# Kernel tuning notes

Hardware: AMD Instinct MI355X
Metric: run time of the kernel (lower is better)

The kernel has to match this reference:

```python
import jax, jax.numpy as jnp
import numpy as np

M, N, DIM = 32, 32, 128
BATCH = 2048
NITER = 100
ALPHA = 0.3
SIGMA = max(M, N) / 2.0


def setup_inputs() -> dict:
    key = jax.random.key(0)
    k1, k2 = jax.random.split(key)
    x = jax.random.normal(k1, (BATCH, DIM), dtype=jnp.float32)
    weights = jax.random.normal(k2, (M * N, DIM), dtype=jnp.float32)
    # Grid locations exactly as in the torch module (meshgrid, ravel, transpose)
    xx, yy = np.meshgrid(np.linspace(0, M - 1, M), np.linspace(0, N - 1, N))
    locations = jnp.asarray(
        np.array((xx.ravel(), yy.ravel())).T.astype(np.int32)
    )  # [mn, 2]
    return {"x": x, "weights": weights, "locations": locations, "it": 5}


def reference(x, weights, locations, it):
    # --- BMU search: pairwise Euclidean distances weights [mn,d] vs x [b,d] ---
    # argmin over squared distances == argmin over cdist (sqrt is monotone)
    w2 = jnp.sum(weights * weights, axis=1)  # [mn]
    x2 = jnp.sum(x * x, axis=1)              # [b]
    d2 = w2[:, None] + x2[None, :] - 2.0 * (weights @ x.T)  # [mn, b]
    bmu_idx = jnp.argmin(d2, axis=0)         # [b]
    bmu_locs = locations[bmu_idx]            # [b, 2]

    # --- linearly decayed learning rate / neighbourhood width ---
    lr_decay = 1.0 - it / NITER
    alpha_op = ALPHA * lr_decay
    sigma_op = SIGMA * lr_decay

    # --- gaussian neighbourhood over grid distances: [mn, b] ---
    locf = locations.astype(jnp.float32)
    bmuf = bmu_locs.astype(jnp.float32)
    bmu_d2 = jnp.sum((locf[:, None, :] - bmuf[None, :, :]) ** 2, axis=2)  # [mn, b]
    lr_op = alpha_op * jnp.exp(-bmu_d2 / (sigma_op * sigma_op))           # [mn, b]

    # --- delta = sum_b lr_op[:, b] * (x[b] - w)  (algebraically reduced) ---
    # == lr_op @ x - rowsum(lr_op) * weights; avoids the [mn, b, d] intermediate
    delta = lr_op @ x - jnp.sum(lr_op, axis=1, keepdims=True) * weights  # [mn, d]
    return weights + delta
```

## Files before the change

kernel.cpp:

```cpp
#include <hip/hip_runtime.h>
#include <stdint.h>

#define DIM   128
#define MN    1024
#define BATCH 2048
#define ALPHA 0.3f
#define SIGMA 16.0f
#define LOG2E 1.44269504088896f

typedef _Float16 half8 __attribute__((ext_vector_type(8)));
typedef _Float16 half4 __attribute__((ext_vector_type(4)));
typedef float    floatx4 __attribute__((ext_vector_type(4)));


__global__ __launch_bounds__(256) void prep_kernel(
    const float* __restrict__ w, float* __restrict__ w2,
    _Float16* __restrict__ wh, _Float16* __restrict__ wl,
    float4* __restrict__ Sq)
{
  const int t = threadIdx.x;
  const int bid = blockIdx.x;
  if (bid < 8) {
    int idx = bid * 256 + t;
    int row = idx >> 1, half = idx & 1;
    int base = row * DIM + half * 64;
    float s = 0.f;
#pragma unroll
    for (int q = 0; q < 16; ++q) {
      float4 v = *reinterpret_cast<const float4*>(&w[base + q * 4]);
      s += v.x * v.x + v.y * v.y + v.z * v.z + v.w * v.w;
      half4 h, l;
      h[0] = (_Float16)v.x; l[0] = (_Float16)(v.x - (float)h[0]);
      h[1] = (_Float16)v.y; l[1] = (_Float16)(v.y - (float)h[1]);
      h[2] = (_Float16)v.z; l[2] = (_Float16)(v.z - (float)h[2]);
      h[3] = (_Float16)v.w; l[3] = (_Float16)(v.w - (float)h[3]);
      *reinterpret_cast<half4*>(&wh[base + q * 4]) = h;
      *reinterpret_cast<half4*>(&wl[base + q * 4]) = l;
    }
    s += __shfl_xor(s, 1);
    if (!half) w2[row] = s;
  } else {
    int i = (bid - 8) * 256 + t;
    Sq[i] = make_float4(0.f, 0.f, 0.f, 0.f);
  }
}

__global__ __launch_bounds__(512) void bmu_scatter_kernel(
    const float* __restrict__ x, const float* __restrict__ w2,
    const _Float16* __restrict__ wh, const _Float16* __restrict__ wl,
    float* __restrict__ S, float* __restrict__ cnt)
{
  __shared__ unsigned long long kb[8][16];
  __shared__ unsigned long long fkey[16];

  const int t    = threadIdx.x;
  const int lane = t & 63;
  const int wv   = t >> 6;
  const int b0   = blockIdx.x * 16;
  const int r    = lane & 15;
  const int q    = lane >> 4;

  half8 Bh[4], Bl[4];
  {
    const float* xr = x + (b0 + r) * DIM + q * 8;
#pragma unroll
    for (int c = 0; c < 4; ++c) {
      float4 v0 = *reinterpret_cast<const float4*>(xr + c * 32);
      float4 v1 = *reinterpret_cast<const float4*>(xr + c * 32 + 4);
      float xs[8] = {v0.x, v0.y, v0.z, v0.w, v1.x, v1.y, v1.z, v1.w};
#pragma unroll
      for (int j = 0; j < 8; ++j) {
        _Float16 h = (_Float16)xs[j];
        Bh[c][j] = h;
        Bl[c][j] = (_Float16)(xs[j] - (float)h);
      }
    }
  }

  unsigned long long kmin = ~0ull;
#pragma unroll 2
  for (int ut = 0; ut < 8; ++ut) {
    const int u0 = wv * 128 + ut * 16;
    const _Float16* wrh = wh + (u0 + r) * DIM + q * 8;
    const _Float16* wrl = wl + (u0 + r) * DIM + q * 8;
    half8 Ah[4], Al[4];
#pragma unroll
    for (int c = 0; c < 4; ++c) {
      Ah[c] = *reinterpret_cast<const half8*>(wrh + c * 32);
      Al[c] = *reinterpret_cast<const half8*>(wrl + c * 32);
    }
    floatx4 acc = {0.f, 0.f, 0.f, 0.f};
#pragma unroll
    for (int c = 0; c < 4; ++c) {
      acc = __builtin_amdgcn_mfma_f32_16x16x32_f16(Ah[c], Bh[c], acc, 0, 0, 0);
      acc = __builtin_amdgcn_mfma_f32_16x16x32_f16(Ah[c], Bl[c], acc, 0, 0, 0);
      acc = __builtin_amdgcn_mfma_f32_16x16x32_f16(Al[c], Bh[c], acc, 0, 0, 0);
    }
    float4 w2q = *reinterpret_cast<const float4*>(&w2[u0 + q * 4]);
    float w2a[4] = {w2q.x, w2q.y, w2q.z, w2q.w};
#pragma unroll
    for (int i = 0; i < 4; ++i) {
      float s = w2a[i] - 2.0f * acc[i];
      unsigned int sb = __float_as_uint(s);
      sb ^= (sb >> 31) ? 0xFFFFFFFFu : 0x80000000u;
      unsigned long long key =
          ((unsigned long long)sb << 32) | (unsigned int)(u0 + q * 4 + i);
      if (key < kmin) kmin = key;
    }
  }
  unsigned long long o;
  o = __shfl_xor(kmin, 16); if (o < kmin) kmin = o;
  o = __shfl_xor(kmin, 32); if (o < kmin) kmin = o;
  if (lane < 16) kb[wv][r] = kmin;
  __syncthreads();
  if (t < 16) {
    unsigned long long m = kb[0][t];
#pragma unroll
    for (int k = 1; k < 8; ++k)
      if (kb[k][t] < m) m = kb[k][t];
    fkey[t] = m;
  }
  __syncthreads();

  {
    int bl = t >> 5, cq = t & 31;
    unsigned int v = (unsigned int)fkey[bl];
    float4 xv = *reinterpret_cast<const float4*>(&x[(b0 + bl) * DIM + cq * 4]);
    float* Sv = S + v * DIM + cq * 4;
    unsafeAtomicAdd(&Sv[0], xv.x);
    unsafeAtomicAdd(&Sv[1], xv.y);
    unsafeAtomicAdd(&Sv[2], xv.z);
    unsafeAtomicAdd(&Sv[3], xv.w);
    if (cq == 0) unsafeAtomicAdd(&cnt[v], 1.0f);
  }
}

__global__ __launch_bounds__(512) void convfinal_kernel(
    const float* __restrict__ S, const float* __restrict__ cnt,
    const float* __restrict__ w, const int* __restrict__ itp,
    float* __restrict__ out)
{
  __shared__ float gxt[64], gyt[64];
  __shared__ __align__(16) float T4[1024][4];
  __shared__ float Tc[1024];

  const int t = threadIdx.x;
  const int q = blockIdx.x;

  const float lr_decay = 1.0f - (float)itp[0] * 0.01f;
  const float alpha_op = ALPHA * lr_decay;
  const float sg       = SIGMA * lr_decay;
  const float c2       = -LOG2E / (sg * sg);

  if (t < 63) {
    float dd = (float)(t - 31);
    float g = __builtin_amdgcn_exp2f(c2 * dd * dd);
    gxt[t] = g;
    gyt[t] = alpha_op * g;
  }
  __syncthreads();

#pragma unroll
  for (int r = 0; r < 2; ++r) {
    int p  = t + 512 * r;
    int vy = p >> 5, ux = p & 31;
    float a0 = 0.f, a1 = 0.f, a2 = 0.f, a3 = 0.f, ac = 0.f;
    const float* Srow = S + (vy * 32) * DIM + q * 4;
    const float* Crow = cnt + vy * 32;
#pragma unroll 4
    for (int vx = 0; vx < 32; ++vx) {
      float g = gxt[ux - vx + 31];
      float4 s4 = *reinterpret_cast<const float4*>(&Srow[vx * DIM]);
      a0 = fmaf(g, s4.x, a0); a1 = fmaf(g, s4.y, a1);
      a2 = fmaf(g, s4.z, a2); a3 = fmaf(g, s4.w, a3);
      ac = fmaf(g, Crow[vx], ac);
    }
    T4[p][0] = a0; T4[p][1] = a1; T4[p][2] = a2; T4[p][3] = a3;
    Tc[p] = ac;
  }
  __syncthreads();

#pragma unroll
  for (int r = 0; r < 2; ++r) {
    int p  = t + 512 * r;
    int uy = p >> 5, ux = p & 31;
    float d0 = 0.f, d1 = 0.f, d2 = 0.f, d3 = 0.f, rs = 0.f;
#pragma unroll 4
    for (int vy = 0; vy < 32; ++vy) {
      float g = gyt[uy - vy + 31];
      float4 t4 = *reinterpret_cast<const float4*>(&T4[vy * 32 + ux][0]);
      d0 = fmaf(g, t4.x, d0); d1 = fmaf(g, t4.y, d1);
      d2 = fmaf(g, t4.z, d2); d3 = fmaf(g, t4.w, d3);
      rs = fmaf(g, Tc[vy * 32 + ux], rs);
    }
    float4 wv = *reinterpret_cast<const float4*>(&w[p * DIM + q * 4]);
    float om = 1.0f - rs;
    float4 o;
    o.x = wv.x * om + d0;
    o.y = wv.y * om + d1;
    o.z = wv.z * om + d2;
    o.w = wv.w * om + d3;
    *reinterpret_cast<float4*>(&out[p * DIM + q * 4]) = o;
  }
}

extern "C" void kernel_launch(void* const* d_in, const int* in_sizes, int n_in,
                              void* d_out, int out_size, void* d_ws, size_t ws_size,
                              hipStream_t stream) {
  const float* x   = (const float*)d_in[0];
  const float* w   = (const float*)d_in[1];
  const int*   itp = (const int*)d_in[3];
  float* out = (float*)d_out;

  char* ws = (char*)d_ws;
  float*     S   = (float*)ws;
  float*     cnt = (float*)(ws + 524288);
  float*     w2  = (float*)(ws + 528384);
  _Float16*  wh  = (_Float16*)(ws + 532480);
  _Float16*  wl  = (_Float16*)(ws + 794624);

  prep_kernel<<<137, 256, 0, stream>>>(w, w2, wh, wl, (float4*)S);
  bmu_scatter_kernel<<<128, 512, 0, stream>>>(x, w2, wh, wl, S, cnt);
  convfinal_kernel<<<32, 512, 0, stream>>>(S, cnt, w, itp, out);
}
```

Measured before the change: 102.4 us.

## Spread neighbourhood convolution over more blocks and double BMU block width

The separable Gaussian convolution kernel is re-partitioned so each block handles one 4-column feature slice and four grid columns. The grid grows from 32 to 256 blocks, and shared memory shrinks to a small per-block tile. The BMU kernel doubles its block size to 1024 threads, so each wave scans half as many units. This is meant to fill more compute units and cut the serial per-thread loop length. In exchange, the convolution now recomputes the x-convolution per column group and uses scalar instead of float4 loads.

```diff
diff --git a/kernel.cpp b/kernel.cpp
--- a/kernel.cpp
+++ b/kernel.cpp
@@ -45,12 +45,12 @@
   }
 }
 
-__global__ __launch_bounds__(512) void bmu_scatter_kernel(
+__global__ __launch_bounds__(1024) void bmu_scatter_kernel(
     const float* __restrict__ x, const float* __restrict__ w2,
     const _Float16* __restrict__ wh, const _Float16* __restrict__ wl,
     float* __restrict__ S, float* __restrict__ cnt)
 {
-  __shared__ unsigned long long kb[8][16];
+  __shared__ unsigned long long kb[16][16];
   __shared__ unsigned long long fkey[16];
 
   const int t    = threadIdx.x;
@@ -79,8 +79,8 @@
 
   unsigned long long kmin = ~0ull;
 #pragma unroll 2
-  for (int ut = 0; ut < 8; ++ut) {
-    const int u0 = wv * 128 + ut * 16;
+  for (int ut = 0; ut < 4; ++ut) {
+    const int u0 = wv * 64 + ut * 16;
     const _Float16* wrh = wh + (u0 + r) * DIM + q * 8;
     const _Float16* wrl = wl + (u0 + r) * DIM + q * 8;
     half8 Ah[4], Al[4];
@@ -116,13 +116,13 @@
   if (t < 16) {
     unsigned long long m = kb[0][t];
 #pragma unroll
-    for (int k = 1; k < 8; ++k)
+    for (int k = 1; k < 16; ++k)
       if (kb[k][t] < m) m = kb[k][t];
     fkey[t] = m;
   }
   __syncthreads();
 
-  {
+  if (t < 512) {
     int bl = t >> 5, cq = t & 31;
     unsigned int v = (unsigned int)fkey[bl];
     float4 xv = *reinterpret_cast<const float4*>(&x[(b0 + bl) * DIM + cq * 4]);
@@ -141,11 +141,17 @@
     float* __restrict__ out)
 {
   __shared__ float gxt[64], gyt[64];
-  __shared__ __align__(16) float T4[1024][4];
-  __shared__ float Tc[1024];
-
-  const int t = threadIdx.x;
-  const int q = blockIdx.x;
+  __shared__ float T1[4][32][4];
+  __shared__ float Tcc[4][32];
+
+  const int t   = threadIdx.x;
+  const int q   = blockIdx.x >> 3;
+  const int uxg = blockIdx.x & 7;
+  const int ui  = t >> 7;
+  const int ux  = uxg * 4 + ui;
+  const int rem = t & 127;
+  const int vy  = rem >> 2;
+  const int j   = rem & 3;
 
   const float lr_decay = 1.0f - (float)itp[0] * 0.01f;
   const float alpha_op = ALPHA * lr_decay;
@@ -160,47 +166,32 @@
   }
   __syncthreads();
 
-#pragma unroll
-  for (int r = 0; r < 2; ++r) {
-    int p  = t + 512 * r;
-    int vy = p >> 5, ux = p & 31;
-    float a0 = 0.f, a1 = 0.f, a2 = 0.f, a3 = 0.f, ac = 0.f;
-    const float* Srow = S + (vy * 32) * DIM + q * 4;
-    const float* Crow = cnt + vy * 32;
-#pragma unroll 4
+  {
+    float a = 0.f, ac = 0.f;
+    const float* Sp = S + (vy * 32) * DIM + q * 4 + j;
+    const float* Cp = cnt + vy * 32;
+#pragma unroll 8
     for (int vx = 0; vx < 32; ++vx) {
       float g = gxt[ux - vx + 31];
-      float4 s4 = *reinterpret_cast<const float4*>(&Srow[vx * DIM]);
-      a0 = fmaf(g, s4.x, a0); a1 = fmaf(g, s4.y, a1);
-      a2 = fmaf(g, s4.z, a2); a3 = fmaf(g, s4.w, a3);
-      ac = fmaf(g, Crow[vx], ac);
-    }
-    T4[p][0] = a0; T4[p][1] = a1; T4[p][2] = a2; T4[p][3] = a3;
-    Tc[p] = ac;
-  }
-  __syncthreads();
-
-#pragma unroll
-  for (int r = 0; r < 2; ++r) {
-    int p  = t + 512 * r;
-    int uy = p >> 5, ux = p & 31;
-    float d0 = 0.f, d1 = 0.f, d2 = 0.f, d3 = 0.f, rs = 0.f;
-#pragma unroll 4
-    for (int vy = 0; vy < 32; ++vy) {
-      float g = gyt[uy - vy + 31];
-      float4 t4 = *reinterpret_cast<const float4*>(&T4[vy * 32 + ux][0]);
-      d0 = fmaf(g, t4.x, d0); d1 = fmaf(g, t4.y, d1);
-      d2 = fmaf(g, t4.z, d2); d3 = fmaf(g, t4.w, d3);
-      rs = fmaf(g, Tc[vy * 32 + ux], rs);
-    }
-    float4 wv = *reinterpret_cast<const float4*>(&w[p * DIM + q * 4]);
-    float om = 1.0f - rs;
-    float4 o;
-    o.x = wv.x * om + d0;
-    o.y = wv.y * om + d1;
-    o.z = wv.z * om + d2;
-    o.w = wv.w * om + d3;
-    *reinterpret_cast<float4*>(&out[p * DIM + q * 4]) = o;
+      a = fmaf(g, Sp[vx * DIM], a);
+      if (j == 0) ac = fmaf(g, Cp[vx], ac);
+    }
+    T1[ui][vy][j] = a;
+    if (j == 0) Tcc[ui][vy] = ac;
+  }
+  __syncthreads();
+
+  {
+    const int uy = vy;
+    float d = 0.f, rs = 0.f;
+#pragma unroll 8
+    for (int v = 0; v < 32; ++v) {
+      float g = gyt[uy - v + 31];
+      d  = fmaf(g, T1[ui][v][j], d);
+      rs = fmaf(g, Tcc[ui][v], rs);
+    }
+    int p = (uy * 32 + ux) * DIM + q * 4 + j;
+    out[p] = w[p] * (1.0f - rs) + d;
   }
 }
 
@@ -220,6 +211,6 @@
   _Float16*  wl  = (_Float16*)(ws + 794624);
 
   prep_kernel<<<137, 256, 0, stream>>>(w, w2, wh, wl, (float4*)S);
-  bmu_scatter_kernel<<<128, 512, 0, stream>>>(x, w2, wh, wl, S, cnt);
-  convfinal_kernel<<<32, 512, 0, stream>>>(S, cnt, w, itp, out);
-}
+  bmu_scatter_kernel<<<128, 1024, 0, stream>>>(x, w2, wh, wl, S, cnt);
+  convfinal_kernel<<<256, 512, 0, stream>>>(S, cnt, w, itp, out);
+}
```

After: 103.9 us. Within noise of the previous version (+1.5%).
